# Performance work log

Hardware: AMD Instinct MI355X
Metric: run time of the kernel (lower is better)

Reference implementation:

```python
import jax, jax.numpy as jnp
import numpy as np

T = 131072      # sequence length (time steps)
IN = 256        # input_dim (MAX_NEURAL_UNITS)
G = 8           # num_dataset_groups
H = 64          # ssm_io_dim (== ssm_dim)
CTX = 8         # context_dim
P = 32          # complex state size = ssm_dim // 2 (conj_sym=True)
NL = 4          # ssm_num_layers
OUT = 2         # output_dim
DT_MIN, DT_MAX = 1e-3, 1e-1


def setup_inputs() -> dict:
    ks = jax.random.split(jax.random.key(0), 16)
    n = lambda i, shape, s=1.0: jax.random.normal(ks[i], shape, dtype=jnp.float32) * s
    return {
        "x": n(0, (T, IN)),
        "group_idx": 3,
        "enc_w": n(1, (G, H - CTX, IN), 1.0 / np.sqrt(IN)),
        "enc_b": n(2, (G, H - CTX), 0.01),
        "ctx_emb": n(3, (G, CTX)),
        "Lambda_re": -0.5 * jnp.abs(n(4, (NL, P))) - 0.1,   # stable (negative real part)
        "Lambda_im": n(5, (NL, P)) * 3.0,
        "B_re": n(6, (NL, P, H), 1.0 / np.sqrt(H)),
        "B_im": n(7, (NL, P, H), 1.0 / np.sqrt(H)),
        "C_re": n(8, (NL, H, P), 1.0 / np.sqrt(P)),
        "C_im": n(9, (NL, H, P), 1.0 / np.sqrt(P)),
        "D": n(10, (NL, H)),
        "log_step": jax.random.uniform(ks[11], (NL, P), jnp.float32, np.log(DT_MIN), np.log(DT_MAX)),
        "norm_scale": jnp.ones((NL, H), jnp.float32),
        "norm_bias": jnp.zeros((NL, H), jnp.float32),
        "glu_w1": n(12, (NL, H, H), 1.0 / np.sqrt(H)),
        "glu_b1": jnp.zeros((NL, H), jnp.float32),
        "glu_w2": n(13, (NL, H, H), 1.0 / np.sqrt(H)),
        "glu_b2": jnp.zeros((NL, H), jnp.float32),
        "dec_w": n(14, (OUT, H), 1.0 / np.sqrt(H)),
        "dec_b": jnp.zeros((OUT,), jnp.float32),
    }


def _s5_scan(Lbar, Bu):
    """Linear recurrence x_k = Lbar * x_{k-1} + Bu_k via parallel associative scan."""
    A = jnp.broadcast_to(Lbar, Bu.shape)  # (T, P) complex

    def binop(a, b):
        a1, u1 = a
        a2, u2 = b
        return a2 * a1, a2 * u1 + u2

    _, xs = jax.lax.associative_scan(binop, (A, Bu))
    return xs  # (T, P) complex


def reference(x, group_idx, enc_w, enc_b, ctx_emb, Lambda_re, Lambda_im, B_re, B_im,
              C_re, C_im, D, log_step, norm_scale, norm_bias,
              glu_w1, glu_b1, glu_w2, glu_b2, dec_w, dec_b):
    # group-routed encoder (lax.switch over per-group Linears == gather of weights)
    h = x @ enc_w[group_idx].T + enc_b[group_idx]                         # (T, H-CTX)
    ctx = jnp.broadcast_to(ctx_emb[group_idx], (h.shape[0], CTX))         # (T, CTX)
    h = jnp.concatenate([h, ctx], axis=1)                                 # (T, H)

    for i in range(NL):  # static layer stack
        skip = h
        # batch-norm over the time axis (training-mode batch statistics)
        mu = jnp.mean(h, axis=0)
        var = jnp.var(h, axis=0)
        hn = (h - mu) * jax.lax.rsqrt(var + 1e-5) * norm_scale[i] + norm_bias[i]

        # ZOH discretisation of diagonal complex SSM
        Lam = jax.lax.complex(Lambda_re[i], Lambda_im[i])                 # (P,)
        dt = jnp.exp(log_step[i])                                         # (P,) step_rescale=1
        Lbar = jnp.exp(Lam * dt)                                          # (P,)
        Bt = jax.lax.complex(B_re[i], B_im[i])                            # (P, H)
        Bbar = (((Lbar - 1.0) / Lam)[:, None]) * Bt                       # (P, H)

        Bu = hn.astype(Bbar.dtype) @ Bbar.T                               # (T, P) complex
        xs = _s5_scan(Lbar, Bu)                                           # (T, P)
        Cm = jax.lax.complex(C_re[i], C_im[i])                            # (H, P)
        y = 2.0 * jnp.real(xs @ Cm.T) + hn * D[i]                         # conj_sym output

        # half-GLU nonlinearity + residual (dropout inactive at inference)
        y = jax.nn.gelu(y)
        y = (y @ glu_w1[i].T + glu_b1[i]) * jax.nn.sigmoid(y @ glu_w2[i].T + glu_b2[i])
        h = skip + y

    return h @ dec_w.T + dec_b                                            # (T, OUT)
```

## Files before the change

### kernel.cpp

```cpp
#include <hip/hip_runtime.h>

#define T_LEN   131072
#define IN_DIM  256
#define HD      64
#define PD      32
#define NLAY    4
#define CHUNK   128
#define NBLK    (T_LEN / CHUNK)
#define ASTR    68

typedef __attribute__((ext_vector_type(8))) short bf16x8;
typedef __attribute__((ext_vector_type(4))) float f32x4;

union FragU { uint4 q; bf16x8 v; };

__device__ __forceinline__ unsigned splitpack(float x) {
    unsigned xb = __float_as_uint(x);
    unsigned hb = (xb + 0x8000u) & 0xffff0000u;
    float lf = x - __uint_as_float(hb);
    unsigned lb = (__float_as_uint(lf) + 0x8000u) >> 16;
    return (hb >> 16) | (lb << 16);
}

__device__ __forceinline__ void packAB(float4 a0, float4 a1, bf16x8& hi, bf16x8& lo) {
    unsigned p0 = splitpack(a0.x), p1 = splitpack(a0.y);
    unsigned p2 = splitpack(a0.z), p3 = splitpack(a0.w);
    unsigned p4 = splitpack(a1.x), p5 = splitpack(a1.y);
    unsigned p6 = splitpack(a1.z), p7 = splitpack(a1.w);
    union { bf16x8 v; unsigned u[4]; } H, L;
    H.u[0] = (p0 & 0xffffu) | (p1 << 16);
    H.u[1] = (p2 & 0xffffu) | (p3 << 16);
    H.u[2] = (p4 & 0xffffu) | (p5 << 16);
    H.u[3] = (p6 & 0xffffu) | (p7 << 16);
    L.u[0] = (p0 >> 16) | (p1 & 0xffff0000u);
    L.u[1] = (p2 >> 16) | (p3 & 0xffff0000u);
    L.u[2] = (p4 >> 16) | (p5 & 0xffff0000u);
    L.u[3] = (p6 >> 16) | (p7 & 0xffff0000u);
    hi = H.v; lo = L.v;
}

#define MFMA3(ACC, AH, AL, BH, BL)                                              \
    ACC = __builtin_amdgcn_mfma_f32_16x16x32_bf16(AH, BH, ACC, 0, 0, 0);        \
    ACC = __builtin_amdgcn_mfma_f32_16x16x32_bf16(AH, BL, ACC, 0, 0, 0);        \
    ACC = __builtin_amdgcn_mfma_f32_16x16x32_bf16(AL, BH, ACC, 0, 0, 0);

__device__ __forceinline__ int kmap(int q, int j) {
    return (j < 4) ? (q * 4 + j) : (16 + q * 4 + (j - 4));
}

__global__ __launch_bounds__(512) void ssm_k0a(
    const float* __restrict__ Lre, const float* __restrict__ Lim,
    const float* __restrict__ logstep,
    float* __restrict__ Lbar, float* __restrict__ Ldt, float* __restrict__ stats)
{
    int tid = threadIdx.x;
    if (tid < NLAY * PD) {
        int l = tid >> 5, p = tid & 31;
        float dt = expf(logstep[l * PD + p]);
        float lr = Lre[l * PD + p], li = Lim[l * PD + p];
        float ldr = lr * dt, ldi = li * dt;
        Ldt[tid * 2] = ldr; Ldt[tid * 2 + 1] = ldi;
        float e = expf(ldr);
        float sn, cs; sincosf(ldi, &sn, &cs);
        Lbar[tid * 2] = e * cs; Lbar[tid * 2 + 1] = e * sn;
    }
    if (tid < NLAY * 128) stats[tid] = 0.0f;
}

__global__ __launch_bounds__(256) void ssm_k0b(
    const float* __restrict__ Lre, const float* __restrict__ Lim,
    const float* __restrict__ logstep,
    const float* __restrict__ Bre, const float* __restrict__ Bim,
    const float* __restrict__ Cre, const float* __restrict__ Cim,
    const float* __restrict__ w1, const float* __restrict__ w2,
    const float* __restrict__ enc_w, const int* __restrict__ gptr,
    unsigned* __restrict__ fragE, unsigned* __restrict__ fragL)
{
    int fi = blockIdx.x * 256 + threadIdx.x;
    if (fi >= 10240) return;
    int g = gptr[0];
    int mat, lay = 0, rem;
    unsigned* outp;
    if (fi < 2048) { mat = 0; rem = fi; outp = fragE + rem * 8; }
    else {
        int t = fi - 2048;
        lay = t / 2048;
        int r2 = t % 2048;
        mat = 1 + r2 / 512;
        rem = r2 % 512;
        outp = fragL + ((size_t)(lay * 4 + (mat - 1)) * 512 + rem) * 8;
    }
    int ks = rem / 256;
    int nt = (rem / 64) & 3;
    int lane = rem & 63;
    int q = lane >> 4;
    int n = nt * 16 + (lane & 15);

    float vals[8];
#pragma unroll
    for (int j = 0; j < 8; ++j) {
        int k = ks * 32 + kmap(q, j);
        float v;
        if (mat == 0) {
            v = (n < 56) ? enc_w[(size_t)(g * 56 + n) * IN_DIM + k] : 0.0f;
        } else if (mat == 1) {
            int p = n >> 1;
            float dt = expf(logstep[lay * PD + p]);
            float lr = Lre[lay * PD + p], li = Lim[lay * PD + p];
            float e = expf(lr * dt);
            float sn, cs; sincosf(li * dt, &sn, &cs);
            float den = lr * lr + li * li;
            float nr = e * cs - 1.0f, ni = e * sn;
            float fr = (nr * lr + ni * li) / den, fimag = (ni * lr - nr * li) / den;
            float br = Bre[(lay * PD + p) * HD + k], bi = Bim[(lay * PD + p) * HD + k];
            v = (n & 1) ? (fr * bi + fimag * br) : (fr * br - fimag * bi);
        } else if (mat == 2) {
            int p = k >> 1;
            v = (k & 1) ? -Cim[((size_t)lay * HD + n) * PD + p]
                        :  Cre[((size_t)lay * HD + n) * PD + p];
        } else if (mat == 3) {
            v = w1[((size_t)lay * HD + n) * HD + k];
        } else {
            v = w2[((size_t)lay * HD + n) * HD + k];
        }
        vals[j] = v;
    }
    unsigned p8[8];
#pragma unroll
    for (int j = 0; j < 8; ++j) p8[j] = splitpack(vals[j]);
#pragma unroll
    for (int w = 0; w < 4; ++w) {
        unsigned p0 = p8[2 * w], p1 = p8[2 * w + 1];
        outp[w]     = (p0 & 0xffffu) | (p1 << 16);
        outp[4 + w] = (p0 >> 16) | (p1 & 0xffff0000u);
    }
}

__global__ __launch_bounds__(64) void ssm_k5_reduce(
    const float* __restrict__ part, float* __restrict__ statsL)
{
    int c = blockIdx.x;
    int lane = threadIdx.x;
    float s = 0.0f;
#pragma unroll
    for (int j = 0; j < 4; ++j) {
        float4 v = *(const float4*)&part[c * 1024 + j * 256 + lane * 4];
        s += v.x + v.y + v.z + v.w;
    }
#pragma unroll
    for (int m = 1; m < 64; m <<= 1) s += __shfl_xor(s, m, 64);
    if (lane == 0) statsL[c] = s;
}

__global__ __launch_bounds__(512, 4) void ssm_k1_encoder(
    const float* __restrict__ x, const int* __restrict__ gptr,
    const unsigned* __restrict__ fragE, const float* __restrict__ enc_b,
    const float* __restrict__ ctx_emb,
    float* __restrict__ h, float* __restrict__ part)
{
    __shared__ float sp1[512], sp2[512];
    int tid = threadIdx.x;
    int l = tid & 63, w = tid >> 6;
    int cq = l >> 4, cr = l & 15;
    int g = gptr[0];
    size_t r0 = (size_t)blockIdx.x * 128;
    int arow = 16 * w + cr;
    const float* xrow = &x[(r0 + arow) * IN_DIM];
    const f32x4 fzero = {0.f, 0.f, 0.f, 0.f};

    float4 cur[16];
#pragma unroll
    for (int kt = 0; kt < 4; ++kt)
#pragma unroll
        for (int ks = 0; ks < 2; ++ks) {
            cur[kt * 4 + 2 * ks]     = *(const float4*)&xrow[kt * 64 + ks * 32 + cq * 4];
            cur[kt * 4 + 2 * ks + 1] = *(const float4*)&xrow[kt * 64 + ks * 32 + cq * 4 + 16];
        }

    f32x4 acc[4];
#pragma unroll
    for (int nt = 0; nt < 4; ++nt) acc[nt] = fzero;

#pragma unroll
    for (int kt = 0; kt < 4; ++kt)
#pragma unroll
        for (int ks = 0; ks < 2; ++ks) {
            bf16x8 ah, al;
            packAB(cur[kt * 4 + 2 * ks], cur[kt * 4 + 2 * ks + 1], ah, al);
            int ksg = kt * 2 + ks;
#pragma unroll
            for (int nt = 0; nt < 4; ++nt) {
                const uint4* wf = (const uint4*)&fragE[((size_t)(ksg * 4 + nt) * 64 + l) * 8];
                FragU BH, BL; BH.q = wf[0]; BL.q = wf[1];
                MFMA3(acc[nt], ah, al, BH.v, BL.v);
            }
        }
#pragma unroll
    for (int nt = 0; nt < 4; ++nt) {
        int ch = nt * 16 + cr;
        float eb = (ch < 56) ? enc_b[g * 56 + ch] : 0.0f;
        bool isctx = (ch >= 56);
        float cv = isctx ? ctx_emb[g * 8 + (ch - 56)] : 0.0f;
        float v1 = 0.0f, v2 = 0.0f;
#pragma unroll
        for (int r = 0; r < 4; ++r) {
            float val = isctx ? cv : (acc[nt][r] + eb);
            h[(r0 + 16 * w + 4 * cq + r) * HD + ch] = val;
            v1 += val; v2 += val * val;
        }
        v1 += __shfl_xor(v1, 16, 64); v2 += __shfl_xor(v2, 16, 64);
        v1 += __shfl_xor(v1, 32, 64); v2 += __shfl_xor(v2, 32, 64);
        if (l < 16) { sp1[w * 64 + ch] = v1; sp2[w * 64 + ch] = v2; }
    }
    __syncthreads();
    if (tid < 64) {
        float s1 = 0.0f, s2 = 0.0f;
#pragma unroll
        for (int ww = 0; ww < 8; ++ww) { s1 += sp1[ww * 64 + tid]; s2 += sp2[ww * 64 + tid]; }
        part[tid * 1024 + blockIdx.x]        = s1;
        part[(64 + tid) * 1024 + blockIdx.x] = s2;
    }
}

__global__ __launch_bounds__(512, 4) void ssm_k2_bu_scan(
    const float* __restrict__ h, const float* __restrict__ stats,
    const float* __restrict__ nscale, const float* __restrict__ nbias,
    const unsigned* __restrict__ fragL, const float* __restrict__ Lbar,
    const float* __restrict__ Ldt,
    unsigned short* __restrict__ xs, float* __restrict__ carry, int lay)
{
    __shared__ __attribute__((aligned(16))) float bf[128 * ASTR];
    __shared__ float lsa[HD], lsb[HD], lld[HD];
    __shared__ float agg[8 * 64], pref[8 * 64];
    int tid = threadIdx.x;
    int l = tid & 63, w = tid >> 6;
    int cq = l >> 4, cr = l & 15;
    size_t r0 = (size_t)blockIdx.x * CHUNK;
    int arow = 16 * w + cr;
    const f32x4 fzero = {0.f, 0.f, 0.f, 0.f};

    if (tid < HD) {
        float s1 = stats[lay * 128 + tid], s2 = stats[lay * 128 + 64 + tid];
        float mu = s1 * (1.0f / T_LEN);
        float var = fmaxf(s2 * (1.0f / T_LEN) - mu * mu, 0.0f);
        float sc = nscale[lay * HD + tid] * rsqrtf(var + 1e-5f);
        lsa[tid] = sc;
        lsb[tid] = nbias[lay * HD + tid] - mu * sc;
        lld[tid] = Ldt[lay * 64 + tid];
    }
    __syncthreads();

    const float* hrowp = &h[(r0 + arow) * HD];
    const unsigned* fB = fragL + (size_t)(lay * 4 + 0) * 4096;
    f32x4 acc[4];
#pragma unroll
    for (int nt = 0; nt < 4; ++nt) acc[nt] = fzero;
#pragma unroll
    for (int ks = 0; ks < 2; ++ks) {
        int k0 = ks * 32 + cq * 4;
        float4 c0 = *(const float4*)&hrowp[k0];
        float4 c1 = *(const float4*)&hrowp[k0 + 16];
        c0.x = c0.x * lsa[k0]      + lsb[k0];
        c0.y = c0.y * lsa[k0 + 1]  + lsb[k0 + 1];
        c0.z = c0.z * lsa[k0 + 2]  + lsb[k0 + 2];
        c0.w = c0.w * lsa[k0 + 3]  + lsb[k0 + 3];
        c1.x = c1.x * lsa[k0 + 16] + lsb[k0 + 16];
        c1.y = c1.y * lsa[k0 + 17] + lsb[k0 + 17];
        c1.z = c1.z * lsa[k0 + 18] + lsb[k0 + 18];
        c1.w = c1.w * lsa[k0 + 19] + lsb[k0 + 19];
        bf16x8 ah, al;
        packAB(c0, c1, ah, al);
#pragma unroll
        for (int nt = 0; nt < 4; ++nt) {
            const uint4* wf = (const uint4*)&fB[((size_t)(ks * 4 + nt) * 64 + l) * 8];
            FragU BH, BL; BH.q = wf[0]; BL.q = wf[1];
            MFMA3(acc[nt], ah, al, BH.v, BL.v);
        }
    }
#pragma unroll
    for (int nt = 0; nt < 4; ++nt)
#pragma unroll
        for (int r = 0; r < 4; ++r)
            bf[(16 * w + 4 * cq + r) * ASTR + nt * 16 + cr] = acc[nt][r];
    __syncthreads();

    {
        int p = l >> 1;
        float Lr = Lbar[(lay * PD + p) * 2];
        float Lj = Lbar[(lay * PD + p) * 2 + 1];
        float csn = (l & 1) ? Lj : -Lj;
        float xv = 0.0f;
        int t0 = 16 * w;
#pragma unroll
        for (int tl = 0; tl < 16; ++tl) {
            float b = bf[(t0 + tl) * ASTR + l];
            float xo = __shfl_xor(xv, 1, 64);
            xv = Lr * xv + csn * xo + b;
            bf[(t0 + tl) * ASTR + l] = xv;
        }
        agg[w * 64 + l] = xv;
    }
    __syncthreads();
    if (w == 0) {
        int p = l >> 1;
        float ldr = lld[2 * p], ldi = lld[2 * p + 1];
        float e16 = __expf(ldr * 16.0f);
        float an = ldi * 16.0f;
        float lcr = e16 * __cosf(an), lci = e16 * __sinf(an);
        float csn16 = (l & 1) ? lci : -lci;
        float pv = 0.0f;
#pragma unroll
        for (int ww = 0; ww < 8; ++ww) {
            pref[ww * 64 + l] = pv;
            float a = agg[ww * 64 + l];
            float po = __shfl_xor(pv, 1, 64);
            pv = lcr * pv + csn16 * po + a;
        }
        carry[(size_t)blockIdx.x * 64 + l] = pv;
    }
    __syncthreads();
    if (w > 0) {
        int p = l >> 1;
        float Lr = Lbar[(lay * PD + p) * 2];
        float Li = Lbar[(lay * PD + p) * 2 + 1];
        float P  = pref[w * 64 + l];
        float Po = __shfl_xor(P, 1, 64);
        float mr = Lr, mi = Li;
        int t0 = 16 * w;
#pragma unroll
        for (int tl = 0; tl < 16; ++tl) {
            float msn = (l & 1) ? mi : -mi;
            bf[(t0 + tl) * ASTR + l] += mr * P + msn * Po;
            float nmr = mr * Lr - mi * Li;
            float nmi = mr * Li + mi * Lr;
            mr = nmr; mi = nmi;
        }
    }
    __syncthreads();
#pragma unroll
    for (int j = 0; j < 2; ++j) {
        unsigned uu[4];
#pragma unroll
        for (int q2 = 0; q2 < 4; ++q2) {
            float a = bf[arow * ASTR + cq * 16 + j * 8 + q2 * 2];
            float b = bf[arow * ASTR + cq * 16 + j * 8 + q2 * 2 + 1];
            unsigned ua = (__float_as_uint(a) + 0x8000u) >> 16;
            unsigned ub = (__float_as_uint(b) + 0x8000u) & 0xffff0000u;
            uu[q2] = ua | ub;
        }
        *(uint4*)&xs[(r0 + arow) * HD + cq * 16 + j * 8] =
            make_uint4(uu[0], uu[1], uu[2], uu[3]);
    }
}

__global__ __launch_bounds__(64) void ssm_k3_carry(
    const float* __restrict__ carry, const float* __restrict__ Ldt,
    float* __restrict__ pc, int lay)
{
    int p = blockIdx.x;
    int lane = threadIdx.x;
    float ldr = Ldt[(lay * PD + p) * 2], ldi = Ldt[(lay * PD + p) * 2 + 1];
    float er = __expf(ldr * (float)CHUNK);
    float an = ldi * (float)CHUNK;
    float lcr = er * __cosf(an), lci = er * __sinf(an);
    float cr[16], ci[16];
#pragma unroll
    for (int j = 0; j < 16; ++j) {
        cr[j] = carry[(size_t)(lane * 16 + j) * 64 + 2 * p];
        ci[j] = carry[(size_t)(lane * 16 + j) * 64 + 2 * p + 1];
    }
    float ur = 0.0f, ui = 0.0f;
#pragma unroll
    for (int j = 0; j < 16; ++j) {
        float nr = lcr * ur - lci * ui + cr[j];
        float ni = lcr * ui + lci * ur + ci[j];
        ur = nr; ui = ni;
    }
    float mr = lcr, mi = lci;
#pragma unroll
    for (int s = 0; s < 4; ++s) { float t = mr * mr - mi * mi; mi = 2.0f * mr * mi; mr = t; }
#pragma unroll
    for (int d = 1; d < 64; d <<= 1) {
        float tr = __shfl_up(ur, d, 64);
        float ti = __shfl_up(ui, d, 64);
        if (lane >= d) { ur = mr * tr - mi * ti + ur; ui = mr * ti + mi * tr + ui; }
        float t = mr * mr - mi * mi; mi = 2.0f * mr * mi; mr = t;
    }
    float pr = __shfl_up(ur, 1, 64), pi = __shfl_up(ui, 1, 64);
    float xr = (lane == 0) ? 0.0f : pr;
    float xi = (lane == 0) ? 0.0f : pi;
#pragma unroll
    for (int j = 0; j < 16; ++j) {
        pc[(size_t)(lane * 16 + j) * 64 + 2 * p]     = xr;
        pc[(size_t)(lane * 16 + j) * 64 + 2 * p + 1] = xi;
        float nr = lcr * xr - lci * xi + cr[j];
        float ni = lcr * xi + lci * xr + ci[j];
        xr = nr; xi = ni;
    }
}

template <bool LAST>
__global__ __launch_bounds__(512, 4) void ssm_k4_out(
    const float* __restrict__ h, const unsigned short* __restrict__ xs,
    const float* __restrict__ pc, const float* __restrict__ stats,
    const float* __restrict__ nscale, const float* __restrict__ nbias,
    const float* __restrict__ Ldt, const unsigned* __restrict__ fragL,
    const float* __restrict__ Dv,
    const float* __restrict__ b1, const float* __restrict__ b2,
    float* __restrict__ hout, float* __restrict__ part,
    const float* __restrict__ dec_w, const float* __restrict__ dec_b,
    float* __restrict__ outp, int lay)
{
    __shared__ __attribute__((aligned(16))) unsigned act[128 * ASTR];
    __shared__ float lsa[HD], lsb[HD], lsd[HD], lpc[HD], lld[HD];
    __shared__ float sp1[512], sp2[512];
    int tid = threadIdx.x;
    int l = tid & 63, w = tid >> 6;
    int cq = l >> 4, cr = l & 15;
    size_t r0 = (size_t)blockIdx.x * CHUNK;
    int arow = 16 * w + cr;
    const f32x4 fzero = {0.f, 0.f, 0.f, 0.f};

    if (tid < HD) {
        float s1 = stats[lay * 128 + tid], s2 = stats[lay * 128 + 64 + tid];
        float mu = s1 * (1.0f / T_LEN);
        float var = fmaxf(s2 * (1.0f / T_LEN) - mu * mu, 0.0f);
        float sc = nscale[lay * HD + tid] * rsqrtf(var + 1e-5f);
        lsa[tid] = sc;
        lsb[tid] = nbias[lay * HD + tid] - mu * sc;
        lsd[tid] = Dv[lay * HD + tid];
        lpc[tid] = pc[(size_t)blockIdx.x * 64 + tid];
        lld[tid] = Ldt[lay * 64 + tid];
    }
    __syncthreads();

    const unsigned* fC = fragL + (size_t)(lay * 4 + 1) * 4096;
    f32x4 yacc[4];
#pragma unroll
    for (int nt = 0; nt < 4; ++nt) yacc[nt] = fzero;
    {
        const unsigned short* xrowp = &xs[(r0 + arow) * HD];
        float tt = (float)(arow + 1);
#pragma unroll
        for (int ks = 0; ks < 2; ++ks) {
            int k0 = ks * 32 + cq * 4;
            uint2 q0 = *(const uint2*)&xrowp[k0];
            uint2 q1 = *(const uint2*)&xrowp[k0 + 16];
            float4 v0 = make_float4(
                __uint_as_float(q0.x << 16), __uint_as_float(q0.x & 0xffff0000u),
                __uint_as_float(q0.y << 16), __uint_as_float(q0.y & 0xffff0000u));
            float4 v1 = make_float4(
                __uint_as_float(q1.x << 16), __uint_as_float(q1.x & 0xffff0000u),
                __uint_as_float(q1.y << 16), __uint_as_float(q1.y & 0xffff0000u));
            {
                float e1 = __expf(lld[k0] * tt), an = lld[k0 + 1] * tt;
                float prr = e1 * __cosf(an), pri = e1 * __sinf(an);
                v0.x += prr * lpc[k0] - pri * lpc[k0 + 1];
                v0.y += prr * lpc[k0 + 1] + pri * lpc[k0];
            }
            {
                float e1 = __expf(lld[k0 + 2] * tt), an = lld[k0 + 3] * tt;
                float prr = e1 * __cosf(an), pri = e1 * __sinf(an);
                v0.z += prr * lpc[k0 + 2] - pri * lpc[k0 + 3];
                v0.w += prr * lpc[k0 + 3] + pri * lpc[k0 + 2];
            }
            {
                float e1 = __expf(lld[k0 + 16] * tt), an = lld[k0 + 17] * tt;
                float prr = e1 * __cosf(an), pri = e1 * __sinf(an);
                v1.x += prr * lpc[k0 + 16] - pri * lpc[k0 + 17];
                v1.y += prr * lpc[k0 + 17] + pri * lpc[k0 + 16];
            }
            {
                float e1 = __expf(lld[k0 + 18] * tt), an = lld[k0 + 19] * tt;
                float prr = e1 * __cosf(an), pri = e1 * __sinf(an);
                v1.z += prr * lpc[k0 + 18] - pri * lpc[k0 + 19];
                v1.w += prr * lpc[k0 + 19] + pri * lpc[k0 + 18];
            }
            bf16x8 ah, al;
            packAB(v0, v1, ah, al);
#pragma unroll
            for (int nt = 0; nt < 4; ++nt) {
                const uint4* wf = (const uint4*)&fC[((size_t)(ks * 4 + nt) * 64 + l) * 8];
                FragU BH, BL; BH.q = wf[0]; BL.q = wf[1];
                MFMA3(yacc[nt], ah, al, BH.v, BL.v);
            }
        }
    }

    float hrow[16];
#pragma unroll
    for (int nt = 0; nt < 4; ++nt) {
        int ch = nt * 16 + cr;
        float sav = lsa[ch], sbv = lsb[ch], dvv = lsd[ch];
#pragma unroll
        for (int r = 0; r < 4; ++r) {
            int row = 16 * w + 4 * cq + r;
            float hv = h[(r0 + row) * HD + ch];
            hrow[nt * 4 + r] = hv;
            float t = 2.0f * yacc[nt][r] + (hv * sav + sbv) * dvv;
            float u2 = 1.5957691216057308f * (t + 0.044715f * t * t * t);
            float gv = t / (1.0f + __expf(-u2));
            act[row * ASTR + ch] = splitpack(gv);
        }
    }
    asm volatile("s_waitcnt lgkmcnt(0)" ::: "memory");

    const unsigned* f1 = fragL + (size_t)(lay * 4 + 2) * 4096;
    const unsigned* f2 = fragL + (size_t)(lay * 4 + 3) * 4096;
    f32x4 uacc[4], sacc[4];
#pragma unroll
    for (int nt = 0; nt < 4; ++nt) { uacc[nt] = fzero; sacc[nt] = fzero; }
#pragma unroll
    for (int ks = 0; ks < 2; ++ks) {
        int col = ks * 32 + 4 * cq;
        uint4 a0 = *(const uint4*)&act[arow * ASTR + col];
        uint4 a1 = *(const uint4*)&act[arow * ASTR + col + 16];
        union { bf16x8 v; unsigned u[4]; } H, L;
        H.u[0] = (a0.x & 0xffffu) | (a0.y << 16);
        H.u[1] = (a0.z & 0xffffu) | (a0.w << 16);
        H.u[2] = (a1.x & 0xffffu) | (a1.y << 16);
        H.u[3] = (a1.z & 0xffffu) | (a1.w << 16);
        L.u[0] = (a0.x >> 16) | (a0.y & 0xffff0000u);
        L.u[1] = (a0.z >> 16) | (a0.w & 0xffff0000u);
        L.u[2] = (a1.x >> 16) | (a1.y & 0xffff0000u);
        L.u[3] = (a1.z >> 16) | (a1.w & 0xffff0000u);
#pragma unroll
        for (int nt = 0; nt < 4; ++nt) {
            const uint4* w1f = (const uint4*)&f1[((size_t)(ks * 4 + nt) * 64 + l) * 8];
            FragU BH1, BL1; BH1.q = w1f[0]; BL1.q = w1f[1];
            MFMA3(uacc[nt], H.v, L.v, BH1.v, BL1.v);
            const uint4* w2f = (const uint4*)&f2[((size_t)(ks * 4 + nt) * 64 + l) * 8];
            FragU BH2, BL2; BH2.q = w2f[0]; BL2.q = w2f[1];
            MFMA3(sacc[nt], H.v, L.v, BH2.v, BL2.v);
        }
    }

    if (LAST) {
        float o0[4] = {0.f, 0.f, 0.f, 0.f}, o1[4] = {0.f, 0.f, 0.f, 0.f};
#pragma unroll
        for (int nt = 0; nt < 4; ++nt) {
            int ch = nt * 16 + cr;
            float bb1 = b1[lay * HD + ch], bb2 = b2[lay * HD + ch];
            float dw0 = dec_w[ch], dw1 = dec_w[64 + ch];
#pragma unroll
            for (int r = 0; r < 4; ++r) {
                float sv = sacc[nt][r] + bb2;
                float sg = 1.0f / (1.0f + __expf(-sv));
                float ho = hrow[nt * 4 + r] + (uacc[nt][r] + bb1) * sg;
                o0[r] += ho * dw0;
                o1[r] += ho * dw1;
            }
        }
#pragma unroll
        for (int r = 0; r < 4; ++r) {
#pragma unroll
            for (int m = 1; m < 16; m <<= 1) {
                o0[r] += __shfl_xor(o0[r], m, 64);
                o1[r] += __shfl_xor(o1[r], m, 64);
            }
        }
        if (cr == 0) {
            float db0 = dec_b[0], db1 = dec_b[1];
#pragma unroll
            for (int r = 0; r < 4; ++r) {
                int row = 16 * w + 4 * cq + r;
                *(float2*)&outp[(r0 + row) * 2] = make_float2(o0[r] + db0, o1[r] + db1);
            }
        }
    } else {
#pragma unroll
        for (int nt = 0; nt < 4; ++nt) {
            int ch = nt * 16 + cr;
            float bb1 = b1[lay * HD + ch], bb2 = b2[lay * HD + ch];
            float v1 = 0.0f, v2 = 0.0f;
#pragma unroll
            for (int r = 0; r < 4; ++r) {
                int row = 16 * w + 4 * cq + r;
                float sv = sacc[nt][r] + bb2;
                float sg = 1.0f / (1.0f + __expf(-sv));
                float ho = hrow[nt * 4 + r] + (uacc[nt][r] + bb1) * sg;
                hout[(r0 + row) * HD + ch] = ho;
                v1 += ho; v2 += ho * ho;
            }
            v1 += __shfl_xor(v1, 16, 64); v2 += __shfl_xor(v2, 16, 64);
            v1 += __shfl_xor(v1, 32, 64); v2 += __shfl_xor(v2, 32, 64);
            if (l < 16) { sp1[w * 64 + ch] = v1; sp2[w * 64 + ch] = v2; }
        }
        __syncthreads();
        if (tid < 64) {
            float s1 = 0.0f, s2 = 0.0f;
#pragma unroll
            for (int ww = 0; ww < 8; ++ww) { s1 += sp1[ww * 64 + tid]; s2 += sp2[ww * 64 + tid]; }
            part[tid * 1024 + blockIdx.x]        = s1;
            part[(64 + tid) * 1024 + blockIdx.x] = s2;
        }
    }
}

extern "C" void kernel_launch(void* const* d_in, const int* in_sizes, int n_in,
                              void* d_out, int out_size, void* d_ws, size_t ws_size,
                              hipStream_t stream)
{
    (void)in_sizes; (void)n_in; (void)out_size; (void)ws_size;
    const float* x     = (const float*)d_in[0];
    const int*   gidx  = (const int*)d_in[1];
    const float* enc_w = (const float*)d_in[2];
    const float* enc_b = (const float*)d_in[3];
    const float* ctx   = (const float*)d_in[4];
    const float* Lre   = (const float*)d_in[5];
    const float* Lim   = (const float*)d_in[6];
    const float* Bre   = (const float*)d_in[7];
    const float* Bim   = (const float*)d_in[8];
    const float* Cre   = (const float*)d_in[9];
    const float* Cim   = (const float*)d_in[10];
    const float* Dv    = (const float*)d_in[11];
    const float* lstep = (const float*)d_in[12];
    const float* nsc   = (const float*)d_in[13];
    const float* nbi   = (const float*)d_in[14];
    const float* w1    = (const float*)d_in[15];
    const float* b1    = (const float*)d_in[16];
    const float* w2    = (const float*)d_in[17];
    const float* b2    = (const float*)d_in[18];
    const float* dw    = (const float*)d_in[19];
    const float* db    = (const float*)d_in[20];
    float* out = (float*)d_out;

    float* ws = (float*)d_ws;
    float* h     = ws;  ws += (size_t)T_LEN * HD;
    unsigned short* xs = (unsigned short*)ws;  ws += (size_t)T_LEN * HD / 2;
    float* carry = ws;  ws += (size_t)NBLK * HD;
    float* pc    = ws;  ws += (size_t)NBLK * HD;
    float* stats = ws;  ws += NLAY * 128;
    float* Lbar  = ws;  ws += NLAY * PD * 2;
    float* Ldt   = ws;  ws += NLAY * PD * 2;
    unsigned* fragE = (unsigned*)ws;  ws += 16384;
    unsigned* fragL = (unsigned*)ws;  ws += 65536;
    float* part  = ws;  ws += 128 * 1024;

    ssm_k0a<<<1, 512, 0, stream>>>(Lre, Lim, lstep, Lbar, Ldt, stats);
    ssm_k0b<<<40, 256, 0, stream>>>(Lre, Lim, lstep, Bre, Bim, Cre, Cim, w1, w2,
                                    enc_w, gidx, fragE, fragL);
    ssm_k1_encoder<<<1024, 512, 0, stream>>>(x, gidx, fragE, enc_b, ctx, h, part);
    ssm_k5_reduce<<<128, 64, 0, stream>>>(part, stats);
    for (int lay = 0; lay < NLAY; ++lay) {
        ssm_k2_bu_scan<<<NBLK, 512, 0, stream>>>(h, stats, nsc, nbi, fragL, Lbar, Ldt,
                                                 xs, carry, lay);
        ssm_k3_carry<<<PD, 64, 0, stream>>>(carry, Ldt, pc, lay);
        if (lay < NLAY - 1) {
            ssm_k4_out<false><<<NBLK, 512, 0, stream>>>(
                h, xs, pc, stats, nsc, nbi, Ldt, fragL, Dv, b1, b2,
                h, part, dw, db, out, lay);
            ssm_k5_reduce<<<128, 64, 0, stream>>>(part, stats + (lay + 1) * 128);
        } else {
            ssm_k4_out<true><<<NBLK, 512, 0, stream>>>(
                h, xs, pc, stats, nsc, nbi, Ldt, fragL, Dv, b1, b2,
                h, part, dw, db, out, lay);
        }
    }
}
```

Measured before the change: 271.6 us.

## Stage global loads and stores through LDS for coalesced row-contiguous access

```diff
diff --git a/kernel.cpp b/kernel.cpp
--- a/kernel.cpp
+++ b/kernel.cpp
@@ -158,6 +158,7 @@
     const float* __restrict__ ctx_emb,
     float* __restrict__ h, float* __restrict__ part)
 {
+    __shared__ __attribute__((aligned(16))) float xt[128 * ASTR];
     __shared__ float sp1[512], sp2[512];
     int tid = threadIdx.x;
     int l = tid & 63, w = tid >> 6;
@@ -165,28 +166,35 @@
     int g = gptr[0];
     size_t r0 = (size_t)blockIdx.x * 128;
     int arow = 16 * w + cr;
-    const float* xrow = &x[(r0 + arow) * IN_DIM];
+    int srow = tid >> 4, sc4 = tid & 15;
     const f32x4 fzero = {0.f, 0.f, 0.f, 0.f};
 
-    float4 cur[16];
-#pragma unroll
-    for (int kt = 0; kt < 4; ++kt)
+    float4 cur[4], nxt[4];
+#pragma unroll
+    for (int it = 0; it < 4; ++it)
+        cur[it] = *(const float4*)&x[(r0 + srow + it * 32) * IN_DIM + sc4 * 4];
+
+    f32x4 acc[4];
+#pragma unroll
+    for (int nt = 0; nt < 4; ++nt) acc[nt] = fzero;
+
+    for (int kt = 0; kt < 4; ++kt) {
+#pragma unroll
+        for (int it = 0; it < 4; ++it)
+            *(float4*)&xt[(srow + it * 32) * ASTR + sc4 * 4] = cur[it];
+        __syncthreads();
+        if (kt < 3) {
+#pragma unroll
+            for (int it = 0; it < 4; ++it)
+                nxt[it] = *(const float4*)&x[(r0 + srow + it * 32) * IN_DIM
+                                             + (kt + 1) * 64 + sc4 * 4];
+        }
 #pragma unroll
         for (int ks = 0; ks < 2; ++ks) {
-            cur[kt * 4 + 2 * ks]     = *(const float4*)&xrow[kt * 64 + ks * 32 + cq * 4];
-            cur[kt * 4 + 2 * ks + 1] = *(const float4*)&xrow[kt * 64 + ks * 32 + cq * 4 + 16];
-        }
-
-    f32x4 acc[4];
-#pragma unroll
-    for (int nt = 0; nt < 4; ++nt) acc[nt] = fzero;
-
-#pragma unroll
-    for (int kt = 0; kt < 4; ++kt)
-#pragma unroll
-        for (int ks = 0; ks < 2; ++ks) {
+            float4 a0 = *(const float4*)&xt[arow * ASTR + ks * 32 + cq * 4];
+            float4 a1 = *(const float4*)&xt[arow * ASTR + ks * 32 + cq * 4 + 16];
             bf16x8 ah, al;
-            packAB(cur[kt * 4 + 2 * ks], cur[kt * 4 + 2 * ks + 1], ah, al);
+            packAB(a0, a1, ah, al);
             int ksg = kt * 2 + ks;
 #pragma unroll
             for (int nt = 0; nt < 4; ++nt) {
@@ -195,6 +203,12 @@
                 MFMA3(acc[nt], ah, al, BH.v, BL.v);
             }
         }
+        __syncthreads();
+        if (kt < 3) {
+#pragma unroll
+            for (int it = 0; it < 4; ++it) cur[it] = nxt[it];
+        }
+    }
 #pragma unroll
     for (int nt = 0; nt < 4; ++nt) {
         int ch = nt * 16 + cr;
@@ -205,7 +219,7 @@
 #pragma unroll
         for (int r = 0; r < 4; ++r) {
             float val = isctx ? cv : (acc[nt][r] + eb);
-            h[(r0 + 16 * w + 4 * cq + r) * HD + ch] = val;
+            xt[(16 * w + 4 * cq + r) * ASTR + ch] = val;
             v1 += val; v2 += val * val;
         }
         v1 += __shfl_xor(v1, 16, 64); v2 += __shfl_xor(v2, 16, 64);
@@ -213,6 +227,11 @@
         if (l < 16) { sp1[w * 64 + ch] = v1; sp2[w * 64 + ch] = v2; }
     }
     __syncthreads();
+#pragma unroll
+    for (int it = 0; it < 4; ++it) {
+        int row = srow + it * 32;
+        *(float4*)&h[(r0 + row) * HD + sc4 * 4] = *(float4*)&xt[row * ASTR + sc4 * 4];
+    }
     if (tid < 64) {
         float s1 = 0.0f, s2 = 0.0f;
 #pragma unroll
@@ -237,7 +256,13 @@
     int cq = l >> 4, cr = l & 15;
     size_t r0 = (size_t)blockIdx.x * CHUNK;
     int arow = 16 * w + cr;
+    int srow = tid >> 4, sc4 = tid & 15;
     const f32x4 fzero = {0.f, 0.f, 0.f, 0.f};
+
+    float4 hq[4];
+#pragma unroll
+    for (int it = 0; it < 4; ++it)
+        hq[it] = *(const float4*)&h[(r0 + srow + it * 32) * HD + sc4 * 4];
 
     if (tid < HD) {
         float s1 = stats[lay * 128 + tid], s2 = stats[lay * 128 + 64 + tid];
@@ -248,9 +273,11 @@
         lsb[tid] = nbias[lay * HD + tid] - mu * sc;
         lld[tid] = Ldt[lay * 64 + tid];
     }
+#pragma unroll
+    for (int it = 0; it < 4; ++it)
+        *(float4*)&bf[(srow + it * 32) * ASTR + sc4 * 4] = hq[it];
     __syncthreads();
 
-    const float* hrowp = &h[(r0 + arow) * HD];
     const unsigned* fB = fragL + (size_t)(lay * 4 + 0) * 4096;
     f32x4 acc[4];
 #pragma unroll
@@ -258,8 +285,8 @@
 #pragma unroll
     for (int ks = 0; ks < 2; ++ks) {
         int k0 = ks * 32 + cq * 4;
-        float4 c0 = *(const float4*)&hrowp[k0];
-        float4 c1 = *(const float4*)&hrowp[k0 + 16];
+        float4 c0 = *(const float4*)&bf[arow * ASTR + k0];
+        float4 c1 = *(const float4*)&bf[arow * ASTR + k0 + 16];
         c0.x = c0.x * lsa[k0]      + lsb[k0];
         c0.y = c0.y * lsa[k0 + 1]  + lsb[k0 + 1];
         c0.z = c0.z * lsa[k0 + 2]  + lsb[k0 + 2];
@@ -277,6 +304,7 @@
             MFMA3(acc[nt], ah, al, BH.v, BL.v);
         }
     }
+    __syncthreads();
 #pragma unroll
     for (int nt = 0; nt < 4; ++nt)
 #pragma unroll
@@ -338,18 +366,17 @@
     }
     __syncthreads();
 #pragma unroll
-    for (int j = 0; j < 2; ++j) {
-        unsigned uu[4];
-#pragma unroll
-        for (int q2 = 0; q2 < 4; ++q2) {
-            float a = bf[arow * ASTR + cq * 16 + j * 8 + q2 * 2];
-            float b = bf[arow * ASTR + cq * 16 + j * 8 + q2 * 2 + 1];
-            unsigned ua = (__float_as_uint(a) + 0x8000u) >> 16;
-            unsigned ub = (__float_as_uint(b) + 0x8000u) & 0xffff0000u;
-            uu[q2] = ua | ub;
-        }
-        *(uint4*)&xs[(r0 + arow) * HD + cq * 16 + j * 8] =
-            make_uint4(uu[0], uu[1], uu[2], uu[3]);
+    for (int it = 0; it < 2; ++it) {
+        int idx = it * 512 + tid;
+        int row = idx >> 3, q8 = idx & 7;
+        float4 fa = *(float4*)&bf[row * ASTR + q8 * 8];
+        float4 fb = *(float4*)&bf[row * ASTR + q8 * 8 + 4];
+        uint4 uu;
+        uu.x = ((__float_as_uint(fa.x) + 0x8000u) >> 16) | ((__float_as_uint(fa.y) + 0x8000u) & 0xffff0000u);
+        uu.y = ((__float_as_uint(fa.z) + 0x8000u) >> 16) | ((__float_as_uint(fa.w) + 0x8000u) & 0xffff0000u);
+        uu.z = ((__float_as_uint(fb.x) + 0x8000u) >> 16) | ((__float_as_uint(fb.y) + 0x8000u) & 0xffff0000u);
+        uu.w = ((__float_as_uint(fb.z) + 0x8000u) >> 16) | ((__float_as_uint(fb.w) + 0x8000u) & 0xffff0000u);
+        *(uint4*)&xs[(r0 + row) * HD + q8 * 8] = uu;
     }
 }
 
@@ -419,7 +446,22 @@
     int cq = l >> 4, cr = l & 15;
     size_t r0 = (size_t)blockIdx.x * CHUNK;
     int arow = 16 * w + cr;
+    int srow = tid >> 4, sc4 = tid & 15;
+    float* actF = (float*)act;
     const f32x4 fzero = {0.f, 0.f, 0.f, 0.f};
+
+    float4 hq[4];
+#pragma unroll
+    for (int it = 0; it < 4; ++it)
+        hq[it] = *(const float4*)&h[(r0 + srow + it * 32) * HD + sc4 * 4];
+    uint2 xq0, xq1, xq2, xq3;
+    {
+        const unsigned short* xrowp = &xs[(r0 + arow) * HD];
+        xq0 = *(const uint2*)&xrowp[cq * 4];
+        xq1 = *(const uint2*)&xrowp[cq * 4 + 16];
+        xq2 = *(const uint2*)&xrowp[32 + cq * 4];
+        xq3 = *(const uint2*)&xrowp[32 + cq * 4 + 16];
+    }
 
     if (tid < HD) {
         float s1 = stats[lay * 128 + tid], s2 = stats[lay * 128 + 64 + tid];
@@ -432,6 +474,9 @@
         lpc[tid] = pc[(size_t)blockIdx.x * 64 + tid];
         lld[tid] = Ldt[lay * 64 + tid];
     }
+#pragma unroll
+    for (int it = 0; it < 4; ++it)
+        *(float4*)&actF[(srow + it * 32) * ASTR + sc4 * 4] = hq[it];
     __syncthreads();
 
     const unsigned* fC = fragL + (size_t)(lay * 4 + 1) * 4096;
@@ -439,13 +484,12 @@
 #pragma unroll
     for (int nt = 0; nt < 4; ++nt) yacc[nt] = fzero;
     {
-        const unsigned short* xrowp = &xs[(r0 + arow) * HD];
         float tt = (float)(arow + 1);
 #pragma unroll
         for (int ks = 0; ks < 2; ++ks) {
             int k0 = ks * 32 + cq * 4;
-            uint2 q0 = *(const uint2*)&xrowp[k0];
-            uint2 q1 = *(const uint2*)&xrowp[k0 + 16];
+            uint2 q0 = ks ? xq2 : xq0;
+            uint2 q1 = ks ? xq3 : xq1;
             float4 v0 = make_float4(
                 __uint_as_float(q0.x << 16), __uint_as_float(q0.x & 0xffff0000u),
                 __uint_as_float(q0.y << 16), __uint_as_float(q0.y & 0xffff0000u));
@@ -495,7 +539,7 @@
 #pragma unroll
         for (int r = 0; r < 4; ++r) {
             int row = 16 * w + 4 * cq + r;
-            float hv = h[(r0 + row) * HD + ch];
+            float hv = actF[row * ASTR + ch];
             hrow[nt * 4 + r] = hv;
             float t = 2.0f * yacc[nt][r] + (hv * sav + sbv) * dvv;
             float u2 = 1.5957691216057308f * (t + 0.044715f * t * t * t);
```

New measurement: 289.0 us. 1.06x slower.
